# Kernel optimization log

Hardware: AMD Instinct MI355X
Metric: run time of the kernel (lower is better)

## Reference

```python
import jax, jax.numpy as jnp
import numpy as np

B, T, C = 2, 2048, 2048
NUM_HEADS, NUM_KV_HEADS, HEAD_DIM = 16, 4, 128
ROPE_THETA = 10000.0
SOFTCAP = 50.0


def sine_table(features, length, min_timescale=1.0, max_timescale=10000.0):
    fraction = jnp.arange(0, features, 2, dtype=jnp.float32) / features
    timescale = min_timescale * (max_timescale / min_timescale) ** fraction
    sinusoid = jnp.arange(length, dtype=jnp.float32)[:, None] / timescale[None, :]
    sinusoid = jnp.concatenate([sinusoid, sinusoid], axis=-1)
    return jnp.sin(sinusoid), jnp.cos(sinusoid)


def rotate_half(x):
    x1, x2 = jnp.split(x, 2, axis=-1)
    return jnp.concatenate([-x2, x1], axis=-1)


def setup_inputs() -> dict:
    key = jax.random.key(0)
    k1, k2, k3, k4, k5 = jax.random.split(key, 5)
    x = jax.random.normal(k1, (B, T, C), dtype=jnp.float32)
    mask = jnp.tril(jnp.ones((T, T), dtype=bool))[None, None]  # causal [1,1,T,T]
    mask = jnp.broadcast_to(mask, (B, 1, T, T))
    std = 0.02
    q_kernel = std * jax.random.normal(k2, (C, NUM_HEADS * HEAD_DIM), dtype=jnp.float32)
    k_kernel = std * jax.random.normal(k3, (C, NUM_KV_HEADS * HEAD_DIM), dtype=jnp.float32)
    v_kernel = std * jax.random.normal(k4, (C, NUM_KV_HEADS * HEAD_DIM), dtype=jnp.float32)
    out_kernel = std * jax.random.normal(k5, (NUM_HEADS * HEAD_DIM, C), dtype=jnp.float32)
    return {"x": x, "mask": mask, "q_kernel": q_kernel, "k_kernel": k_kernel,
            "v_kernel": v_kernel, "out_kernel": out_kernel}


def reference(x, mask, q_kernel, k_kernel, v_kernel, out_kernel):
    _, t, c = x.shape
    r = NUM_HEADS // NUM_KV_HEADS  # GQA group size
    qp = q_kernel.reshape(c, r, NUM_KV_HEADS, HEAD_DIM)
    kp = k_kernel.reshape(c, NUM_KV_HEADS, HEAD_DIM)
    vp = v_kernel.reshape(c, NUM_KV_HEADS, HEAD_DIM)
    op = out_kernel.reshape(r, NUM_KV_HEADS, HEAD_DIM, c)
    q = jnp.einsum('bsm,mrhk->brhsk', x, qp)   # [B,r,h,T,hd]
    k = jnp.einsum('bdm,mhk->bhdk', x, kp)     # [B,h,T,hd]
    v = jnp.einsum('bdm,mhv->bhdv', x, vp)     # [B,h,T,hd]
    sin, cos = sine_table(HEAD_DIM, t, max_timescale=ROPE_THETA)  # [T,hd]
    q = q * cos + rotate_half(q) * sin  # broadcast over leading dims (time at -2)
    k = k * cos + rotate_half(k) * sin
    scale = jax.lax.rsqrt(jnp.array(HEAD_DIM, dtype=x.dtype))
    qk = jnp.einsum('brhsk,bhdk->brhsd', q, k) * scale  # [B,r,h,T,T]
    qk = jnp.tanh(qk / SOFTCAP) * SOFTCAP  # logit softcap
    m = jnp.expand_dims(mask, axis=1)  # [B,1,1,T,T]
    qk = jax.nn.softmax(qk.astype(jnp.float32), where=m).astype(x.dtype)
    qkv = jnp.einsum('brhsd,bhdv->brhsv', qk, v)
    out = jnp.einsum('brhsv,rhvm->bsm', qkv, op)
    return out
```

## Files before the change

kernel.cpp:

```cpp
#include <hip/hip_runtime.h>
#include <hip/hip_bf16.h>

typedef __hip_bfloat16 bf16;
typedef __attribute__((ext_vector_type(8))) short bf16x8;
typedef __attribute__((ext_vector_type(4))) short bf16x4;
typedef __attribute__((ext_vector_type(4))) float f32x4;

#define BATCH 2
#define SEQ 2048
#define CDIM 2048
#define NH 16
#define NKV 4
#define HD 128
#define NQKV 3072

__device__ __forceinline__ float tof(float x)  { return x; }
__device__ __forceinline__ float tof(bf16 x)   { return __bfloat162float(x); }
__device__ __forceinline__ void  stf(float* p, float v) { *p = v; }
__device__ __forceinline__ void  stf(bf16* p,  float v) { *p = __float2bfloat16(v); }

__device__ __forceinline__ void gl_lds16(const bf16* g, bf16* l) {
    typedef const __attribute__((address_space(1))) unsigned int* gp_t;
    typedef __attribute__((address_space(3))) unsigned int* lp_t;
    __builtin_amdgcn_global_load_lds((gp_t)g, (lp_t)l, 16, 0, 0);
}

__device__ __forceinline__ f32x4 mfma16x16x16_bf16(bf16x4 a, bf16x4 b, f32x4 c) {
#if __has_builtin(__builtin_amdgcn_mfma_f32_16x16x16bf16_1k)
    return __builtin_amdgcn_mfma_f32_16x16x16bf16_1k(a, b, c, 0, 0, 0);
#else
    asm volatile("v_mfma_f32_16x16x16_bf16 %0, %1, %2, %0"
                 : "+v"(c) : "v"(a), "v"(b));
    return c;
#endif
}

__device__ __forceinline__ float fast_exp2(float x) {
#if __has_builtin(__builtin_amdgcn_exp2f)
    return __builtin_amdgcn_exp2f(x);
#else
    return exp2f(x);
#endif
}

__global__ __launch_bounds__(256) void f2b_kernel(const float* __restrict__ in,
                                                  bf16* __restrict__ out, int n4)
{
    int i = blockIdx.x * 256 + threadIdx.x;
    if (i >= n4) return;
    float4 v = *(const float4*)&in[(size_t)i * 4];
    bf16 o[4] = {__float2bfloat16(v.x), __float2bfloat16(v.y),
                 __float2bfloat16(v.z), __float2bfloat16(v.w)};
    *(ushort4*)&out[(size_t)i * 4] = *(ushort4*)o;
}

__global__ __launch_bounds__(256) void transpose_f2b_kernel(
    const float* __restrict__ in, bf16* __restrict__ out, int R, int Cn)
{
    __shared__ float tile[64][65];
    const int r0 = blockIdx.y * 64, c0 = blockIdx.x * 64;
    for (int f = threadIdx.x; f < 4096; f += 256) {
        int r = f >> 6, c = f & 63;
        tile[r][c] = in[(size_t)(r0 + r) * Cn + c0 + c];
    }
    __syncthreads();
    for (int f = threadIdx.x; f < 4096; f += 256) {
        int r = f >> 6, c = f & 63;
        out[(size_t)(c0 + r) * R + r0 + c] = __float2bfloat16(tile[c][r]);
    }
}

__global__ __launch_bounds__(256) void vtrans_kernel(
    const bf16* __restrict__ in, bf16* __restrict__ out)
{
    __shared__ bf16 tile[64][65];
    const int b = blockIdx.z;
    const int t0 = blockIdx.y * 64, c0 = blockIdx.x * 64;
    for (int f = threadIdx.x; f < 4096; f += 256) {
        int r = f >> 6, c = f & 63;
        tile[r][c] = in[(size_t)(b * SEQ + t0 + r) * (NKV * HD) + c0 + c];
    }
    __syncthreads();
    for (int f = threadIdx.x; f < 4096; f += 256) {
        int r = f >> 6, c = f & 63;
        out[(size_t)(b * NKV * HD + c0 + r) * SEQ + t0 + c] = tile[c][r];
    }
}

__global__ __launch_bounds__(256) void gemm_qkv_kernel(
    const bf16* __restrict__ A, const bf16* __restrict__ Bt,
    bf16* __restrict__ Qr, bf16* __restrict__ Kr, bf16* __restrict__ Vr,
    int M, int K)
{
    __shared__ __align__(16) bf16 As[128 * 32];
    __shared__ __align__(16) bf16 Bs[128 * 32];

    const int tid = threadIdx.x;
    const int lane = tid & 63;
    const int wave = tid >> 6;
    const int m0 = blockIdx.y * 128;
    const int n0 = blockIdx.x * 128;
    const int wm = (wave >> 1) * 64;
    const int wn = (wave & 1) * 64;
    const int quad = lane >> 4;
    const int l16 = lane & 15;

    const int srow = tid >> 2;
    const int scol = (tid & 3) * 8;
    const bf16* Ag0 = A  + (size_t)(m0 + srow) * K + scol;
    const bf16* Ag1 = A  + (size_t)(m0 + srow + 64) * K + scol;
    const bf16* Bg0 = Bt + (size_t)(n0 + srow) * K + scol;
    const bf16* Bg1 = Bt + (size_t)(n0 + srow + 64) * K + scol;

    f32x4 acc[4][4];
#pragma unroll
    for (int mi = 0; mi < 4; ++mi)
#pragma unroll
        for (int ni = 0; ni < 4; ++ni)
            acc[mi][ni] = (f32x4){0.f, 0.f, 0.f, 0.f};

    for (int kt = 0; kt < K; kt += 32) {
        __syncthreads();
        gl_lds16(Ag0 + kt, &As[tid * 8]);
        gl_lds16(Ag1 + kt, &As[2048 + tid * 8]);
        gl_lds16(Bg0 + kt, &Bs[tid * 8]);
        gl_lds16(Bg1 + kt, &Bs[2048 + tid * 8]);
        __syncthreads();

        bf16x8 a[4], b[4];
#pragma unroll
        for (int mi = 0; mi < 4; ++mi)
            a[mi] = *(const bf16x8*)&As[(wm + mi * 16 + l16) * 32 + quad * 8];
#pragma unroll
        for (int ni = 0; ni < 4; ++ni)
            b[ni] = *(const bf16x8*)&Bs[(wn + ni * 16 + l16) * 32 + quad * 8];
#pragma unroll
        for (int mi = 0; mi < 4; ++mi)
#pragma unroll
            for (int ni = 0; ni < 4; ++ni)
                acc[mi][ni] = __builtin_amdgcn_mfma_f32_16x16x32_bf16(
                    a[mi], b[ni], acc[mi][ni], 0, 0, 0);
    }

    bf16* Cp; int Nst, cbase;
    if (n0 < 2048)      { Cp = Qr; Nst = 2048; cbase = n0; }
    else if (n0 < 2560) { Cp = Kr; Nst = 512;  cbase = n0 - 2048; }
    else                { Cp = Vr; Nst = 512;  cbase = n0 - 2560; }

#pragma unroll
    for (int mi = 0; mi < 4; ++mi)
#pragma unroll
        for (int ni = 0; ni < 4; ++ni) {
            int col = cbase + wn + ni * 16 + l16;
#pragma unroll
            for (int r = 0; r < 4; ++r) {
                int row = m0 + wm + mi * 16 + quad * 4 + r;
                Cp[(size_t)row * Nst + col] = __float2bfloat16(acc[mi][ni][r]);
            }
        }
}

template <typename TC>
__global__ __launch_bounds__(256) void gemm_mfma_bt(
    const bf16* __restrict__ A, const bf16* __restrict__ Bt, TC* __restrict__ C,
    int M, int N, int K)
{
    __shared__ __align__(16) bf16 As[128 * 32];
    __shared__ __align__(16) bf16 Bs[128 * 32];

    const int tid = threadIdx.x;
    const int lane = tid & 63;
    const int wave = tid >> 6;
    const int m0 = blockIdx.y * 128;
    const int n0 = blockIdx.x * 128;
    const int wm = (wave >> 1) * 64;
    const int wn = (wave & 1) * 64;
    const int quad = lane >> 4;
    const int l16 = lane & 15;

    const int srow = tid >> 2;
    const int scol = (tid & 3) * 8;
    const bf16* Ag0 = A  + (size_t)(m0 + srow) * K + scol;
    const bf16* Ag1 = A  + (size_t)(m0 + srow + 64) * K + scol;
    const bf16* Bg0 = Bt + (size_t)(n0 + srow) * K + scol;
    const bf16* Bg1 = Bt + (size_t)(n0 + srow + 64) * K + scol;

    f32x4 acc[4][4];
#pragma unroll
    for (int mi = 0; mi < 4; ++mi)
#pragma unroll
        for (int ni = 0; ni < 4; ++ni)
            acc[mi][ni] = (f32x4){0.f, 0.f, 0.f, 0.f};

    for (int kt = 0; kt < K; kt += 32) {
        __syncthreads();
        gl_lds16(Ag0 + kt, &As[tid * 8]);
        gl_lds16(Ag1 + kt, &As[2048 + tid * 8]);
        gl_lds16(Bg0 + kt, &Bs[tid * 8]);
        gl_lds16(Bg1 + kt, &Bs[2048 + tid * 8]);
        __syncthreads();

        bf16x8 a[4], b[4];
#pragma unroll
        for (int mi = 0; mi < 4; ++mi)
            a[mi] = *(const bf16x8*)&As[(wm + mi * 16 + l16) * 32 + quad * 8];
#pragma unroll
        for (int ni = 0; ni < 4; ++ni)
            b[ni] = *(const bf16x8*)&Bs[(wn + ni * 16 + l16) * 32 + quad * 8];
#pragma unroll
        for (int mi = 0; mi < 4; ++mi)
#pragma unroll
            for (int ni = 0; ni < 4; ++ni)
                acc[mi][ni] = __builtin_amdgcn_mfma_f32_16x16x32_bf16(
                    a[mi], b[ni], acc[mi][ni], 0, 0, 0);
    }

#pragma unroll
    for (int mi = 0; mi < 4; ++mi)
#pragma unroll
        for (int ni = 0; ni < 4; ++ni) {
            int col = n0 + wn + ni * 16 + l16;
#pragma unroll
            for (int r = 0; r < 4; ++r) {
                int row = m0 + wm + mi * 16 + quad * 4 + r;
                stf(&C[(size_t)row * N + col], acc[mi][ni][r]);
            }
        }
}

__global__ __launch_bounds__(256) void rope_kernel(bf16* __restrict__ data,
                                                   int ncols, int total_pairs)
{
    int idx = blockIdx.x * 256 + threadIdx.x;
    if (idx >= total_pairs) return;
    int half = ncols >> 1;
    int row = idx / half;
    int p = idx - row * half;
    int head = p >> 6;
    int i = p & 63;
    int t = row & (SEQ - 1);
    float inv_ts = expf(-(float)i * 0.14391156831212787f);
    float angle = (float)t * inv_ts;
    float s, c;
    sincosf(angle, &s, &c);
    size_t base = (size_t)row * ncols + head * 128 + i;
    float x1 = __bfloat162float(data[base]);
    float x2 = __bfloat162float(data[base + 64]);
    data[base]      = __float2bfloat16(x1 * c - x2 * s);
    data[base + 64] = __float2bfloat16(x2 * c + x1 * s);
}

__global__ __launch_bounds__(256, 3) void attn_mfma5_kernel(
    const bf16* __restrict__ Q, const bf16* __restrict__ K,
    const bf16* __restrict__ Vt, bf16* __restrict__ Att)
{
    __shared__ __align__(16) char smem[32768];
    bf16* Ks  = (bf16*)smem;
    bf16* Vts = (bf16*)(smem + 16384);

    const int tid = threadIdx.x;
    const int lane = tid & 63;
    const int w = tid >> 6;
    const int hs = w >> 1;
    const int qw = w & 1;
    const int quad = lane >> 4;
    const int l16 = lane & 15;
    const int bh = blockIdx.y;
    const int b   = bh >> 3;
    const int kvh = (bh >> 1) & 3;
    const int pr  = bh & 1;
    const int hq  = kvh + 4 * (pr * 2 + hs);
    const int qt = (gridDim.x - 1) - blockIdx.x;
    const int q0 = qt * 64 + qw * 32;

    bf16x8 qf[2][4];
#pragma unroll
    for (int g = 0; g < 2; ++g) {
        size_t qrow = (size_t)(b * SEQ + q0 + g * 16 + l16) * (NH * HD) + hq * HD;
#pragma unroll
        for (int kk = 0; kk < 4; ++kk)
            qf[g][kk] = *(const bf16x8*)&Q[qrow + kk * 32 + quad * 8];
    }

    const bf16* Kb = K  + (size_t)(b * SEQ) * (NKV * HD) + kvh * HD;
    const bf16* Vb = Vt + (size_t)((b * NKV + kvh) * HD) * SEQ;

    f32x4 O[2][8];
#pragma unroll
    for (int g = 0; g < 2; ++g)
#pragma unroll
        for (int dj = 0; dj < 8; ++dj) O[g][dj] = (f32x4){0.f, 0.f, 0.f, 0.f};
    float lsum[2] = {0.f, 0.f};

    const int srowK = tid >> 4;
    const int sgcK  = (tid & 15) ^ srowK;
    const int srowV = tid >> 3;
    const int sgcV  = (tid & 7) ^ (srowV & 7);

    const int ntiles = qt + 1;
    for (int jt = 0; jt < ntiles; ++jt) {
        const int j0 = jt * 64;
        __syncthreads();
#pragma unroll
        for (int c = 0; c < 4; ++c) {
            gl_lds16(Kb + (size_t)(j0 + c * 16 + srowK) * (NKV * HD) + sgcK * 8,
                     Ks + c * 2048 + tid * 8);
            gl_lds16(Vb + (size_t)(c * 32 + srowV) * SEQ + j0 + sgcV * 8,
                     Vts + c * 2048 + tid * 8);
        }
        __syncthreads();

        const bool diag = (jt == qt);
#pragma unroll
        for (int half = 0; half < 2; ++half) {
            f32x4 sacc[2][2];
#pragma unroll
            for (int mt = 0; mt < 2; ++mt) {
#pragma unroll
                for (int g = 0; g < 2; ++g) sacc[mt][g] = (f32x4){0.f, 0.f, 0.f, 0.f};
                const int krow = (half * 32 + mt * 16 + l16) * 128;
#pragma unroll
                for (int kk = 0; kk < 4; ++kk) {
                    bf16x8 kf = *(const bf16x8*)&Ks[krow + (((kk * 4 + quad) ^ l16) * 8)];
#pragma unroll
                    for (int g = 0; g < 2; ++g)
                        sacc[mt][g] = __builtin_amdgcn_mfma_f32_16x16x32_bf16(
                            kf, qf[g][kk], sacc[mt][g], 0, 0, 0);
                }
            }

            bf16x4 pf[2][2];
#pragma unroll
            for (int mt = 0; mt < 2; ++mt)
#pragma unroll
                for (int g = 0; g < 2; ++g) {
                    bf16 pb[4];
#pragma unroll
                    for (int r = 0; r < 4; ++r) {
                        float u = sacc[mt][g][r];
                        float t2 = u * u;
                        float num = fmaf(t2, 9.96274e-4f, 8607.814f);
                        float den = fmaf(t2, 0.0703125f, 67500.f);
                        float s2 = u * num * __builtin_amdgcn_rcpf(den);
                        float p = fast_exp2(s2);
                        if (diag) {
                            int kl = half * 32 + mt * 16 + quad * 4 + r;
                            int ql = qw * 32 + g * 16 + l16;
                            p = (kl <= ql) ? p : 0.f;
                        }
                        lsum[g] += p;
                        pb[r] = __float2bfloat16(p);
                    }
                    pf[mt][g] = *(bf16x4*)pb;
                }

#pragma unroll
            for (int dj = 0; dj < 8; ++dj) {
                const int vrow = (dj * 16 + l16) * 64;
                const int dl7 = l16 & 7;
#pragma unroll
                for (int mt = 0; mt < 2; ++mt) {
                    int c16 = half * 4 + mt * 2 + (quad >> 1);
                    bf16x4 vf = *(const bf16x4*)&Vts[vrow + ((c16 ^ dl7) << 3)
                                                     + (quad & 1) * 4];
#pragma unroll
                    for (int g = 0; g < 2; ++g)
                        O[g][dj] = mfma16x16x16_bf16(vf, pf[mt][g], O[g][dj]);
                }
            }
        }
    }

#pragma unroll
    for (int g = 0; g < 2; ++g) {
        float v = lsum[g];
        v += __shfl_xor(v, 16);
        v += __shfl_xor(v, 32);
        float inv = 1.f / v;
        size_t obase = (size_t)(b * SEQ + q0 + g * 16 + l16) * (NH * HD) + hq * HD;
#pragma unroll
        for (int dj = 0; dj < 8; ++dj) {
            bf16 ob[4];
#pragma unroll
            for (int r = 0; r < 4; ++r)
                ob[r] = __float2bfloat16(O[g][dj][r] * inv);
            *(ushort4*)&Att[obase + dj * 16 + quad * 4] = *(ushort4*)ob;
        }
    }
}

extern "C" void kernel_launch(void* const* d_in, const int* in_sizes, int n_in,
                              void* d_out, int out_size, void* d_ws, size_t ws_size,
                              hipStream_t stream) {
    const float* x        = (const float*)d_in[0];
    const float* q_kernel = (const float*)d_in[2];
    const float* k_kernel = (const float*)d_in[3];
    const float* v_kernel = (const float*)d_in[4];
    const float* o_kernel = (const float*)d_in[5];
    float* out = (float*)d_out;

    const int M = BATCH * SEQ;
    char* ws = (char*)d_ws;
    bf16* xb   = (bf16*)ws;
    bf16* Att  = xb;
    bf16* wT   = (bf16*)(ws + 16777216);
    bf16* wTq  = wT;
    bf16* wTk  = wT + (size_t)2048 * 2048;
    bf16* wTv  = wT + (size_t)2560 * 2048;
    bf16* woT  = wT;
    bf16* Vt_g = (bf16*)(ws + 25165824);
    bf16* Qr   = (bf16*)(ws + 29360128);
    bf16* Kr   = (bf16*)(ws + 46137344);
    bf16* Vr   = (bf16*)(ws + 50331648);

    f2b_kernel<<<(M * CDIM / 4 + 255) / 256, 256, 0, stream>>>(x, xb, M * CDIM / 4);
    transpose_f2b_kernel<<<dim3((NH * HD) / 64, CDIM / 64), 256, 0, stream>>>(
        q_kernel, wTq, CDIM, NH * HD);
    transpose_f2b_kernel<<<dim3((NKV * HD) / 64, CDIM / 64), 256, 0, stream>>>(
        k_kernel, wTk, CDIM, NKV * HD);
    transpose_f2b_kernel<<<dim3((NKV * HD) / 64, CDIM / 64), 256, 0, stream>>>(
        v_kernel, wTv, CDIM, NKV * HD);

    gemm_qkv_kernel<<<dim3(NQKV / 128, M / 128), 256, 0, stream>>>(
        xb, wT, Qr, Kr, Vr, M, CDIM);

    transpose_f2b_kernel<<<dim3(CDIM / 64, CDIM / 64), 256, 0, stream>>>(
        o_kernel, woT, CDIM, CDIM);

    {
        int pairs_q = M * (NH * HD / 2);
        rope_kernel<<<pairs_q / 256, 256, 0, stream>>>(Qr, NH * HD, pairs_q);
        int pairs_k = M * (NKV * HD / 2);
        rope_kernel<<<pairs_k / 256, 256, 0, stream>>>(Kr, NKV * HD, pairs_k);
    }

    vtrans_kernel<<<dim3((NKV * HD) / 64, SEQ / 64, BATCH), 256, 0, stream>>>(Vr, Vt_g);

    attn_mfma5_kernel<<<dim3(SEQ / 64, BATCH * NKV * 2), 256, 0, stream>>>(
        Qr, Kr, Vt_g, Att);

    gemm_mfma_bt<float><<<dim3(CDIM / 128, M / 128), 256, 0, stream>>>(
        Att, woT, out, M, CDIM, CDIM);
}
```

Measured before the change: 400.6 us.

## Halve attention query tile per block to double grid parallelism

Each warp now handles 16 query rows instead of 32, so a block covers 32 queries and the grid doubles along the sequence axis. The diagonal-tile mask and the tile count are adjusted to the new 32-row tiling while K/V still load in 64-key tiles. This cuts per-thread registers and gives more blocks to spread the causal workload. In exchange, each K/V tile loaded into LDS is reused by half as many queries, which doubles K/V load traffic, and the diagonal tile wastes more masked work.

Measured after the change: 395.8 us. Within noise of the previous version (-1.2%).

```diff
diff --git a/kernel.cpp b/kernel.cpp
--- a/kernel.cpp
+++ b/kernel.cpp
@@ -250,7 +250,7 @@
     data[base + 64] = __float2bfloat16(x2 * c + x1 * s);
 }
 
-__global__ __launch_bounds__(256, 3) void attn_mfma5_kernel(
+__global__ __launch_bounds__(256, 3) void attn_mfma6_kernel(
     const bf16* __restrict__ Q, const bf16* __restrict__ K,
     const bf16* __restrict__ Vt, bf16* __restrict__ Att)
 {
@@ -271,33 +271,31 @@
     const int pr  = bh & 1;
     const int hq  = kvh + 4 * (pr * 2 + hs);
     const int qt = (gridDim.x - 1) - blockIdx.x;
-    const int q0 = qt * 64 + qw * 32;
-
-    bf16x8 qf[2][4];
-#pragma unroll
-    for (int g = 0; g < 2; ++g) {
-        size_t qrow = (size_t)(b * SEQ + q0 + g * 16 + l16) * (NH * HD) + hq * HD;
+    const int q0 = qt * 32 + qw * 16;
+
+    bf16x8 qf[4];
+    {
+        size_t qrow = (size_t)(b * SEQ + q0 + l16) * (NH * HD) + hq * HD;
 #pragma unroll
         for (int kk = 0; kk < 4; ++kk)
-            qf[g][kk] = *(const bf16x8*)&Q[qrow + kk * 32 + quad * 8];
+            qf[kk] = *(const bf16x8*)&Q[qrow + kk * 32 + quad * 8];
     }
 
     const bf16* Kb = K  + (size_t)(b * SEQ) * (NKV * HD) + kvh * HD;
     const bf16* Vb = Vt + (size_t)((b * NKV + kvh) * HD) * SEQ;
 
-    f32x4 O[2][8];
-#pragma unroll
-    for (int g = 0; g < 2; ++g)
-#pragma unroll
-        for (int dj = 0; dj < 8; ++dj) O[g][dj] = (f32x4){0.f, 0.f, 0.f, 0.f};
-    float lsum[2] = {0.f, 0.f};
+    f32x4 O[8];
+#pragma unroll
+    for (int dj = 0; dj < 8; ++dj) O[dj] = (f32x4){0.f, 0.f, 0.f, 0.f};
+    float lsum = 0.f;
 
     const int srowK = tid >> 4;
     const int sgcK  = (tid & 15) ^ srowK;
     const int srowV = tid >> 3;
     const int sgcV  = (tid & 7) ^ (srowV & 7);
 
-    const int ntiles = qt + 1;
+    const int ntiles = (qt >> 1) + 1;
+    const int qsel = (qt & 1) * 32 + qw * 16 + l16;
     for (int jt = 0; jt < ntiles; ++jt) {
         const int j0 = jt * 64;
         __syncthreads();
@@ -310,49 +308,43 @@
         }
         __syncthreads();
 
-        const bool diag = (jt == qt);
+        const bool diag = (jt == (qt >> 1));
 #pragma unroll
         for (int half = 0; half < 2; ++half) {
-            f32x4 sacc[2][2];
+            f32x4 sacc[2];
 #pragma unroll
             for (int mt = 0; mt < 2; ++mt) {
-#pragma unroll
-                for (int g = 0; g < 2; ++g) sacc[mt][g] = (f32x4){0.f, 0.f, 0.f, 0.f};
+                sacc[mt] = (f32x4){0.f, 0.f, 0.f, 0.f};
                 const int krow = (half * 32 + mt * 16 + l16) * 128;
 #pragma unroll
                 for (int kk = 0; kk < 4; ++kk) {
                     bf16x8 kf = *(const bf16x8*)&Ks[krow + (((kk * 4 + quad) ^ l16) * 8)];
-#pragma unroll
-                    for (int g = 0; g < 2; ++g)
-                        sacc[mt][g] = __builtin_amdgcn_mfma_f32_16x16x32_bf16(
-                            kf, qf[g][kk], sacc[mt][g], 0, 0, 0);
+                    sacc[mt] = __builtin_amdgcn_mfma_f32_16x16x32_bf16(
+                        kf, qf[kk], sacc[mt], 0, 0, 0);
                 }
             }
 
-            bf16x4 pf[2][2];
-#pragma unroll
-            for (int mt = 0; mt < 2; ++mt)
-#pragma unroll
-                for (int g = 0; g < 2; ++g) {
-                    bf16 pb[4];
-#pragma unroll
-                    for (int r = 0; r < 4; ++r) {
-                        float u = sacc[mt][g][r];
-                        float t2 = u * u;
-                        float num = fmaf(t2, 9.96274e-4f, 8607.814f);
-                        float den = fmaf(t2, 0.0703125f, 67500.f);
-                        float s2 = u * num * __builtin_amdgcn_rcpf(den);
-                        float p = fast_exp2(s2);
-                        if (diag) {
-                            int kl = half * 32 + mt * 16 + quad * 4 + r;
-                            int ql = qw * 32 + g * 16 + l16;
-                            p = (kl <= ql) ? p : 0.f;
-                        }
-                        lsum[g] += p;
-                        pb[r] = __float2bfloat16(p);
+            bf16x4 pf[2];
+#pragma unroll
+            for (int mt = 0; mt < 2; ++mt) {
+                bf16 pb[4];
+#pragma unroll
+                for (int r = 0; r < 4; ++r) {
+                    float u = sacc[mt][r];
+                    float t2 = u * u;
+                    float num = fmaf(t2, 9.96274e-4f, 8607.814f);
+                    float den = fmaf(t2, 0.0703125f, 67500.f);
+                    float s2 = u * num * __builtin_amdgcn_rcpf(den);
+                    float p = fast_exp2(s2);
+                    if (diag) {
+                        int kl = half * 32 + mt * 16 + quad * 4 + r;
+                        p = (kl <= qsel) ? p : 0.f;
                     }
-                    pf[mt][g] = *(bf16x4*)pb;
+                    lsum += p;
+                    pb[r] = __float2bfloat16(p);
                 }
+                pf[mt] = *(bf16x4*)pb;
+            }
 
 #pragma unroll
             for (int dj = 0; dj < 8; ++dj) {
@@ -363,27 +355,24 @@
                     int c16 = half * 4 + mt * 2 + (quad >> 1);
                     bf16x4 vf = *(const bf16x4*)&Vts[vrow + ((c16 ^ dl7) << 3)
                                                      + (quad & 1) * 4];
-#pragma unroll
-                    for (int g = 0; g < 2; ++g)
-                        O[g][dj] = mfma16x16x16_bf16(vf, pf[mt][g], O[g][dj]);
+                    O[dj] = mfma16x16x16_bf16(vf, pf[mt], O[dj]);
                 }
             }
         }
     }
 
-#pragma unroll
-    for (int g = 0; g < 2; ++g) {
-        float v = lsum[g];
+    {
+        float v = lsum;
         v += __shfl_xor(v, 16);
         v += __shfl_xor(v, 32);
         float inv = 1.f / v;
-        size_t obase = (size_t)(b * SEQ + q0 + g * 16 + l16) * (NH * HD) + hq * HD;
+        size_t obase = (size_t)(b * SEQ + q0 + l16) * (NH * HD) + hq * HD;
 #pragma unroll
         for (int dj = 0; dj < 8; ++dj) {
             bf16 ob[4];
 #pragma unroll
             for (int r = 0; r < 4; ++r)
-                ob[r] = __float2bfloat16(O[g][dj][r] * inv);
+                ob[r] = __float2bfloat16(O[dj][r] * inv);
             *(ushort4*)&Att[obase + dj * 16 + quad * 4] = *(ushort4*)ob;
         }
     }
@@ -436,7 +425,7 @@
 
     vtrans_kernel<<<dim3((NKV * HD) / 64, SEQ / 64, BATCH), 256, 0, stream>>>(Vr, Vt_g);
 
-    attn_mfma5_kernel<<<dim3(SEQ / 64, BATCH * NKV * 2), 256, 0, stream>>>(
+    attn_mfma6_kernel<<<dim3(SEQ / 32, BATCH * NKV * 2), 256, 0, stream>>>(
         Qr, Kr, Vt_g, Att);
 
     gemm_mfma_bt<float><<<dim3(CDIM / 128, M / 128), 256, 0, stream>>>(
```
